# Performance work log

Measured on AMD Instinct MI355X. Metric: run time of the kernel, lower is better.

Reference implementation:

```python
import jax, jax.numpy as jnp
import numpy as np

B, K, D, H = 16, 256, 256, 128

def setup_inputs() -> dict:
    key = jax.random.key(0)
    k1, k2, k3 = jax.random.split(key, 3)
    x = jax.random.normal(k1, (B, K, D), dtype=jnp.float32)
    # Linear(2D, H): weight stored as (2D, H) for x @ W convention
    W1 = jax.random.normal(k2, (2 * D, H), dtype=jnp.float32) * (1.0 / np.sqrt(2 * D))
    b1 = jnp.zeros((H,), dtype=jnp.float32)
    W2 = jax.random.normal(k3, (H, D), dtype=jnp.float32) * (1.0 / np.sqrt(H))
    b2 = jnp.zeros((D,), dtype=jnp.float32)
    return {"x": x, "W1": W1, "b1": b1, "W2": W2, "b2": b2}

def reference(x, W1, b1, W2, b2):
    # Original: for each i, concat([x_i broadcast, x_j]) -> Linear -> ReLU -> Linear -> mean_j, + residual.
    # Split the first Linear over the concat: W1 = [W1a; W1b], so
    # pre-act(i,j) = x_i @ W1a + x_j @ W1b + b1  (avoids materializing the concat).
    D_ = x.shape[-1]
    W1a, W1b = W1[:D_], W1[D_:]
    a = jnp.einsum('bkd,dh->bkh', x, W1a)            # B x K x H (query side)
    b = jnp.einsum('bkd,dh->bkh', x, W1b)            # B x K x H (key side)
    h = jax.nn.relu(a[:, :, None, :] + b[:, None, :, :] + b1)  # B x K x K x H
    mh = h.mean(axis=2)                               # mean over j; Linear commutes with mean
    out = jnp.einsum('bkh,hd->bkd', mh, W2) + b2      # B x K x D
    return out + x
```

## Files before the change

### kernel.cpp

```cpp
#include <hip/hip_runtime.h>

typedef __attribute__((ext_vector_type(8))) short bf16x8;
typedef __attribute__((ext_vector_type(4))) float f32x4;

union FragU { uint4 q; bf16x8 h; };

__device__ __forceinline__ unsigned short f2bf(float f) {
  unsigned u = __float_as_uint(f);
  u += 0x7FFFu + ((u >> 16) & 1u);
  return (unsigned short)(u >> 16);
}
__device__ __forceinline__ unsigned pack2(float lo, float hi) {
  return (unsigned)f2bf(lo) | ((unsigned)f2bf(hi) << 16);
}

__global__ __launch_bounds__(256) void kX(
    const float* __restrict__ x, const float* __restrict__ W1,
    const float* __restrict__ W2, uint4* __restrict__ xbf,
    uint4* __restrict__ w1f, uint4* __restrict__ w2f)
{
  const int u = blockIdx.x * 256 + threadIdx.x;
  if (u < 131072) {
    const int l = u & 63, c = (u >> 6) & 7, t = (u >> 9) & 15, b = u >> 13;
    const int fr = l & 15, fq = l >> 4;
    const float* p = x + (size_t)((b * 16 + t) * 16 + fr) * 256 + c * 32 + fq * 8;
    float4 va = *(const float4*)p;
    float4 vb = *(const float4*)(p + 4);
    xbf[u] = make_uint4(pack2(va.x, va.y), pack2(va.z, va.w),
                        pack2(vb.x, vb.y), pack2(vb.z, vb.w));
  } else if (u < 139264) {
    const int u2 = u - 131072;
    const int l = u2 & 63, c = (u2 >> 6) & 7, hc = u2 >> 9;
    const int fr = l & 15, fq = l >> 4;
    const float* p = W1 + (size_t)((fr >= 8) ? 256 : 0) * 128 +
                     (size_t)(c * 32 + fq * 8) * 128 + hc * 8 + (fr & 7);
    float v[8];
#pragma unroll
    for (int j = 0; j < 8; ++j) v[j] = p[(size_t)j * 128];
    w1f[u2] = make_uint4(pack2(v[0], v[1]), pack2(v[2], v[3]),
                         pack2(v[4], v[5]), pack2(v[6], v[7]));
  } else if (u < 143360) {
    const int u3 = u - 139264;
    const int l = u3 & 63, c = (u3 >> 6) & 3, dg = u3 >> 8;
    const int fr = l & 15, fq = l >> 4;
    const float* p = W2 + (size_t)(c * 32 + fq * 8) * 256 + dg * 16 + fr;
    float v[8];
#pragma unroll
    for (int j = 0; j < 8; ++j) v[j] = p[(size_t)j * 256];
    w2f[u3] = make_uint4(pack2(v[0], v[1]), pack2(v[2], v[3]),
                         pack2(v[4], v[5]), pack2(v[6], v[7]));
  }
}

__global__ __launch_bounds__(1024) void kA(
    const uint4* __restrict__ xbf, const uint4* __restrict__ w1f,
    const float* __restrict__ b1, uint4* __restrict__ mf)
{
  __shared__ float Cs[8][260];
  __shared__ float As[8][260];
  __shared__ float PB[8][260];

  const int tid = threadIdx.x, lane = tid & 63, wv = tid >> 6;
  const int b = blockIdx.x, hc = blockIdx.y;
  const int fr = lane & 15, fq = lane >> 4;

  FragU afr[8];
#pragma unroll
  for (int c = 0; c < 8; ++c) afr[c].q = w1f[(hc * 8 + c) * 64 + lane];

  float b1v[4];
#pragma unroll
  for (int g = 0; g < 4; ++g)
    b1v[g] = (fq >= 2) ? b1[hc * 8 + (fq - 2) * 4 + g] : 0.f;

  {
    const int t = wv;
    f32x4 acc = {0.f, 0.f, 0.f, 0.f};
#pragma unroll
    for (int c = 0; c < 8; ++c) {
      FragU bfr;
      bfr.q = xbf[((size_t)(b * 16 + t) * 8 + c) * 64 + lane];
      acc = __builtin_amdgcn_mfma_f32_16x16x32_bf16(afr[c].h, bfr.h, acc, 0, 0, 0);
    }
    const int m = t * 16 + fr;
    if (fq < 2) {
#pragma unroll
      for (int g = 0; g < 4; ++g) As[fq * 4 + g][m] = acc[g];
    } else {
#pragma unroll
      for (int g = 0; g < 4; ++g) Cs[(fq - 2) * 4 + g][m] = acc[g] + b1v[g];
    }
  }
  __syncthreads();

  const int hp = wv & 7, kh = wv >> 3;
  const float a0 = As[hp][lane],       a1 = As[hp][64 + lane];
  const float a2 = As[hp][128 + lane], a3 = As[hp][192 + lane];

  float sumC = 0.f;
  if (kh == 0) {
    float4 s4 = *(const float4*)&Cs[hp][lane * 4];
    sumC = (s4.x + s4.y) + (s4.z + s4.w);
#pragma unroll
    for (int off = 32; off >= 1; off >>= 1) sumC += __shfl_xor(sumC, off, 64);
  }

  float s0a = 0.f, s0b = 0.f, s1a = 0.f, s1b = 0.f;
  float s2a = 0.f, s2b = 0.f, s3a = 0.f, s3b = 0.f;
  const int u0 = kh * 32;
#pragma unroll 8
  for (int u = 0; u < 32; ++u) {
    float4 c = *(const float4*)&Cs[hp][(u0 + u) * 4];
    s0a += fabsf(a0 + c.x); s0b += fabsf(a0 + c.y);
    s0a += fabsf(a0 + c.z); s0b += fabsf(a0 + c.w);
    s1a += fabsf(a1 + c.x); s1b += fabsf(a1 + c.y);
    s1a += fabsf(a1 + c.z); s1b += fabsf(a1 + c.w);
    s2a += fabsf(a2 + c.x); s2b += fabsf(a2 + c.y);
    s2a += fabsf(a2 + c.z); s2b += fabsf(a2 + c.w);
    s3a += fabsf(a3 + c.x); s3b += fabsf(a3 + c.y);
    s3a += fabsf(a3 + c.z); s3b += fabsf(a3 + c.w);
  }

  if (kh == 1) {
    PB[hp][lane]       = s0a + s0b;
    PB[hp][64 + lane]  = s1a + s1b;
    PB[hp][128 + lane] = s2a + s2b;
    PB[hp][192 + lane] = s3a + s3b;
  }
  __syncthreads();

  if (kh == 0) {
    As[hp][lane]       = (256.f * a0 + sumC + (s0a + s0b) + PB[hp][lane])       * (1.f / 512.f);
    As[hp][64 + lane]  = (256.f * a1 + sumC + (s1a + s1b) + PB[hp][64 + lane])  * (1.f / 512.f);
    As[hp][128 + lane] = (256.f * a2 + sumC + (s2a + s2b) + PB[hp][128 + lane]) * (1.f / 512.f);
    As[hp][192 + lane] = (256.f * a3 + sumC + (s3a + s3b) + PB[hp][192 + lane]) * (1.f / 512.f);
  }
  __syncthreads();

  if (tid < 256) {
    const int fr2 = tid & 15, T = tid >> 4;
    uint4 o = make_uint4(pack2(As[0][tid], As[1][tid]), pack2(As[2][tid], As[3][tid]),
                         pack2(As[4][tid], As[5][tid]), pack2(As[6][tid], As[7][tid]));
    mf[((size_t)(b * 16 + T) * 4 + (hc >> 2)) * 64 + (hc & 3) * 16 + fr2] = o;
  }
}

__global__ __launch_bounds__(256) void kB(
    const uint4* __restrict__ mf, const uint4* __restrict__ w2f,
    const float* __restrict__ b2, const float* __restrict__ x,
    float* __restrict__ out)
{
  const int tid = threadIdx.x, lane = tid & 63, wu = tid >> 6;
  const int mt = blockIdx.x;
  const int dg = blockIdx.y * 4 + wu;
  const int fr = lane & 15, fq = lane >> 4;

  f32x4 acc = {0.f, 0.f, 0.f, 0.f};
#pragma unroll
  for (int c = 0; c < 4; ++c) {
    FragU a, bb;
    a.q  = mf[((size_t)mt * 4 + c) * 64 + lane];
    bb.q = w2f[((size_t)dg * 4 + c) * 64 + lane];
    acc = __builtin_amdgcn_mfma_f32_16x16x32_bf16(a.h, bb.h, acc, 0, 0, 0);
  }

  const int d = dg * 16 + fr;
  const float bv = b2[d];
#pragma unroll
  for (int g = 0; g < 4; ++g) {
    const int m = mt * 16 + fq * 4 + g;
    const size_t o = (size_t)m * 256 + d;
    out[o] = acc[g] + bv + x[o];
  }
}

extern "C" void kernel_launch(void* const* d_in, const int* in_sizes, int n_in,
                              void* d_out, int out_size, void* d_ws, size_t ws_size,
                              hipStream_t stream) {
  const float* x  = (const float*)d_in[0];
  const float* W1 = (const float*)d_in[1];
  const float* b1 = (const float*)d_in[2];
  const float* W2 = (const float*)d_in[3];
  const float* b2 = (const float*)d_in[4];
  float* out = (float*)d_out;

  char* ws = (char*)d_ws;
  uint4* xbf = (uint4*)ws;
  uint4* w1f = (uint4*)(ws + (2u << 20));
  uint4* w2f = (uint4*)(ws + (2u << 20) + (128u << 10));
  uint4* mf  = (uint4*)(ws + (2u << 20) + (192u << 10));

  kX<<<560, 256, 0, stream>>>(x, W1, W2, xbf, w1f, w2f);
  kA<<<dim3(16, 16), 1024, 0, stream>>>(xbf, w1f, b1, mf);
  kB<<<dim3(256, 4), 256, 0, stream>>>(mf, w2f, b2, x, out);
}
```

Before: 25.60 us.

## Fuse bf16 conversion into consumer kernels and drop the pre-pass kernel

Removes the separate conversion kernel. kA now loads fp32 x for its batch, converts it with the hardware packed bf16 convert instruction, and stores it in a swizzled 128KB LDS tile. It also converts its W1 fragments directly from global memory, and kB converts its W2 fragments the same way. The goal is to cut one launch and the intermediate workspace round-trip. The cost is that each of the 16 hc blocks per batch re-reads and re-converts the full fp32 x slice, and the large LDS footprint limits occupancy. The pairwise abs-sum loop also switches to inline-asm packed f32 adds.

```diff
diff --git a/kernel.cpp b/kernel.cpp
--- a/kernel.cpp
+++ b/kernel.cpp
@@ -2,93 +2,73 @@
 
 typedef __attribute__((ext_vector_type(8))) short bf16x8;
 typedef __attribute__((ext_vector_type(4))) float f32x4;
+typedef __attribute__((ext_vector_type(2))) float f32x2;
 
 union FragU { uint4 q; bf16x8 h; };
 
-__device__ __forceinline__ unsigned short f2bf(float f) {
-  unsigned u = __float_as_uint(f);
-  u += 0x7FFFu + ((u >> 16) & 1u);
-  return (unsigned short)(u >> 16);
-}
-__device__ __forceinline__ unsigned pack2(float lo, float hi) {
-  return (unsigned)f2bf(lo) | ((unsigned)f2bf(hi) << 16);
-}
-
-__global__ __launch_bounds__(256) void kX(
-    const float* __restrict__ x, const float* __restrict__ W1,
-    const float* __restrict__ W2, uint4* __restrict__ xbf,
-    uint4* __restrict__ w1f, uint4* __restrict__ w2f)
-{
-  const int u = blockIdx.x * 256 + threadIdx.x;
-  if (u < 131072) {
-    const int l = u & 63, c = (u >> 6) & 7, t = (u >> 9) & 15, b = u >> 13;
-    const int fr = l & 15, fq = l >> 4;
-    const float* p = x + (size_t)((b * 16 + t) * 16 + fr) * 256 + c * 32 + fq * 8;
-    float4 va = *(const float4*)p;
-    float4 vb = *(const float4*)(p + 4);
-    xbf[u] = make_uint4(pack2(va.x, va.y), pack2(va.z, va.w),
-                        pack2(vb.x, vb.y), pack2(vb.z, vb.w));
-  } else if (u < 139264) {
-    const int u2 = u - 131072;
-    const int l = u2 & 63, c = (u2 >> 6) & 7, hc = u2 >> 9;
-    const int fr = l & 15, fq = l >> 4;
-    const float* p = W1 + (size_t)((fr >= 8) ? 256 : 0) * 128 +
-                     (size_t)(c * 32 + fq * 8) * 128 + hc * 8 + (fr & 7);
-    float v[8];
-#pragma unroll
-    for (int j = 0; j < 8; ++j) v[j] = p[(size_t)j * 128];
-    w1f[u2] = make_uint4(pack2(v[0], v[1]), pack2(v[2], v[3]),
-                         pack2(v[4], v[5]), pack2(v[6], v[7]));
-  } else if (u < 143360) {
-    const int u3 = u - 139264;
-    const int l = u3 & 63, c = (u3 >> 6) & 3, dg = u3 >> 8;
-    const int fr = l & 15, fq = l >> 4;
-    const float* p = W2 + (size_t)(c * 32 + fq * 8) * 256 + dg * 16 + fr;
-    float v[8];
-#pragma unroll
-    for (int j = 0; j < 8; ++j) v[j] = p[(size_t)j * 256];
-    w2f[u3] = make_uint4(pack2(v[0], v[1]), pack2(v[2], v[3]),
-                         pack2(v[4], v[5]), pack2(v[6], v[7]));
-  }
+__device__ __forceinline__ unsigned cvt_pk(float lo, float hi) {
+  unsigned r;
+  asm("v_cvt_pk_bf16_f32 %0, %1, %2" : "=v"(r) : "v"(lo), "v"(hi));
+  return r;
 }
 
 __global__ __launch_bounds__(1024) void kA(
-    const uint4* __restrict__ xbf, const uint4* __restrict__ w1f,
+    const float* __restrict__ x, const float* __restrict__ W1,
     const float* __restrict__ b1, uint4* __restrict__ mf)
 {
+  __shared__ __align__(16) unsigned short xs[256 * 256];
+  __shared__ float As[8][260];
   __shared__ float Cs[8][260];
-  __shared__ float As[8][260];
   __shared__ float PB[8][260];
 
   const int tid = threadIdx.x, lane = tid & 63, wv = tid >> 6;
   const int b = blockIdx.x, hc = blockIdx.y;
   const int fr = lane & 15, fq = lane >> 4;
 
+#pragma unroll
+  for (int i = 0; i < 16; ++i) {
+    const int idx = i * 1024 + tid;
+    const int row = idx >> 6, u = idx & 63;
+    float4 v = *(const float4*)&x[(size_t)(b * 256 + row) * 256 + u * 4];
+    uint2 hv = make_uint2(cvt_pk(v.x, v.y), cvt_pk(v.z, v.w));
+    *(uint2*)&xs[row * 256 + (u ^ ((row & 7) << 1)) * 4] = hv;
+  }
+
+  const float* __restrict__ wp =
+      W1 + (size_t)((fr >= 8) ? 256 : 0) * 128 + hc * 8 + (fr & 7);
   FragU afr[8];
 #pragma unroll
-  for (int c = 0; c < 8; ++c) afr[c].q = w1f[(hc * 8 + c) * 64 + lane];
+  for (int c = 0; c < 8; ++c) {
+    float v[8];
+#pragma unroll
+    for (int j = 0; j < 8; ++j) v[j] = wp[(size_t)(c * 32 + fq * 8 + j) * 128];
+    afr[c].q = make_uint4(cvt_pk(v[0], v[1]), cvt_pk(v[2], v[3]),
+                          cvt_pk(v[4], v[5]), cvt_pk(v[6], v[7]));
+  }
 
   float b1v[4];
 #pragma unroll
   for (int g = 0; g < 4; ++g)
     b1v[g] = (fq >= 2) ? b1[hc * 8 + (fq - 2) * 4 + g] : 0.f;
 
+  __syncthreads();
+
   {
-    const int t = wv;
+    const int mrow = wv * 16 + fr;
+    const int swz = (mrow & 7) << 1;
     f32x4 acc = {0.f, 0.f, 0.f, 0.f};
 #pragma unroll
     for (int c = 0; c < 8; ++c) {
-      FragU bfr;
-      bfr.q = xbf[((size_t)(b * 16 + t) * 8 + c) * 64 + lane];
-      acc = __builtin_amdgcn_mfma_f32_16x16x32_bf16(afr[c].h, bfr.h, acc, 0, 0, 0);
+      const int pu = (c * 8 + fq * 2) ^ swz;
+      bf16x8 bfr = *(const bf16x8*)&xs[mrow * 256 + pu * 4];
+      acc = __builtin_amdgcn_mfma_f32_16x16x32_bf16(afr[c].h, bfr, acc, 0, 0, 0);
     }
-    const int m = t * 16 + fr;
     if (fq < 2) {
 #pragma unroll
-      for (int g = 0; g < 4; ++g) As[fq * 4 + g][m] = acc[g];
+      for (int g = 0; g < 4; ++g) As[fq * 4 + g][mrow] = acc[g];
     } else {
 #pragma unroll
-      for (int g = 0; g < 4; ++g) Cs[(fq - 2) * 4 + g][m] = acc[g] + b1v[g];
+      for (int g = 0; g < 4; ++g) Cs[(fq - 2) * 4 + g][mrow] = acc[g] + b1v[g];
     }
   }
   __syncthreads();
@@ -105,48 +85,57 @@
     for (int off = 32; off >= 1; off >>= 1) sumC += __shfl_xor(sumC, off, 64);
   }
 
-  float s0a = 0.f, s0b = 0.f, s1a = 0.f, s1b = 0.f;
-  float s2a = 0.f, s2b = 0.f, s3a = 0.f, s3b = 0.f;
+  const f32x2 aa0 = {a0, a0}, aa1 = {a1, a1}, aa2 = {a2, a2}, aa3 = {a3, a3};
+  float s0l = 0.f, s0h = 0.f, s1l = 0.f, s1h = 0.f;
+  float s2l = 0.f, s2h = 0.f, s3l = 0.f, s3h = 0.f;
   const int u0 = kh * 32;
+
+#define PROW(aa, sl, sh)                                                   \
+  {                                                                        \
+    f32x2 t0, t1;                                                          \
+    asm("v_pk_add_f32 %0, %1, %2" : "=v"(t0) : "v"(aa), "v"(c01));         \
+    asm("v_pk_add_f32 %0, %1, %2" : "=v"(t1) : "v"(aa), "v"(c23));         \
+    sl += __builtin_fabsf(t0.x); sh += __builtin_fabsf(t0.y);              \
+    sl += __builtin_fabsf(t1.x); sh += __builtin_fabsf(t1.y);              \
+  }
+
 #pragma unroll 8
   for (int u = 0; u < 32; ++u) {
-    float4 c = *(const float4*)&Cs[hp][(u0 + u) * 4];
-    s0a += fabsf(a0 + c.x); s0b += fabsf(a0 + c.y);
-    s0a += fabsf(a0 + c.z); s0b += fabsf(a0 + c.w);
-    s1a += fabsf(a1 + c.x); s1b += fabsf(a1 + c.y);
-    s1a += fabsf(a1 + c.z); s1b += fabsf(a1 + c.w);
-    s2a += fabsf(a2 + c.x); s2b += fabsf(a2 + c.y);
-    s2a += fabsf(a2 + c.z); s2b += fabsf(a2 + c.w);
-    s3a += fabsf(a3 + c.x); s3b += fabsf(a3 + c.y);
-    s3a += fabsf(a3 + c.z); s3b += fabsf(a3 + c.w);
+    float4 c4 = *(const float4*)&Cs[hp][(u0 + u) * 4];
+    f32x2 c01 = {c4.x, c4.y}, c23 = {c4.z, c4.w};
+    PROW(aa0, s0l, s0h)
+    PROW(aa1, s1l, s1h)
+    PROW(aa2, s2l, s2h)
+    PROW(aa3, s3l, s3h)
   }
+#undef PROW
 
   if (kh == 1) {
-    PB[hp][lane]       = s0a + s0b;
-    PB[hp][64 + lane]  = s1a + s1b;
-    PB[hp][128 + lane] = s2a + s2b;
-    PB[hp][192 + lane] = s3a + s3b;
+    PB[hp][lane]       = s0l + s0h;
+    PB[hp][64 + lane]  = s1l + s1h;
+    PB[hp][128 + lane] = s2l + s2h;
+    PB[hp][192 + lane] = s3l + s3h;
   }
   __syncthreads();
 
   if (kh == 0) {
-    As[hp][lane]       = (256.f * a0 + sumC + (s0a + s0b) + PB[hp][lane])       * (1.f / 512.f);
-    As[hp][64 + lane]  = (256.f * a1 + sumC + (s1a + s1b) + PB[hp][64 + lane])  * (1.f / 512.f);
-    As[hp][128 + lane] = (256.f * a2 + sumC + (s2a + s2b) + PB[hp][128 + lane]) * (1.f / 512.f);
-    As[hp][192 + lane] = (256.f * a3 + sumC + (s3a + s3b) + PB[hp][192 + lane]) * (1.f / 512.f);
+    As[hp][lane]       = (256.f * a0 + sumC + (s0l + s0h) + PB[hp][lane])       * (1.f / 512.f);
+    As[hp][64 + lane]  = (256.f * a1 + sumC + (s1l + s1h) + PB[hp][64 + lane])  * (1.f / 512.f);
+    As[hp][128 + lane] = (256.f * a2 + sumC + (s2l + s2h) + PB[hp][128 + lane]) * (1.f / 512.f);
+    As[hp][192 + lane] = (256.f * a3 + sumC + (s3l + s3h) + PB[hp][192 + lane]) * (1.f / 512.f);
   }
   __syncthreads();
 
   if (tid < 256) {
     const int fr2 = tid & 15, T = tid >> 4;
-    uint4 o = make_uint4(pack2(As[0][tid], As[1][tid]), pack2(As[2][tid], As[3][tid]),
-                         pack2(As[4][tid], As[5][tid]), pack2(As[6][tid], As[7][tid]));
+    uint4 o = make_uint4(cvt_pk(As[0][tid], As[1][tid]), cvt_pk(As[2][tid], As[3][tid]),
+                         cvt_pk(As[4][tid], As[5][tid]), cvt_pk(As[6][tid], As[7][tid]));
     mf[((size_t)(b * 16 + T) * 4 + (hc >> 2)) * 64 + (hc & 3) * 16 + fr2] = o;
   }
 }
 
 __global__ __launch_bounds__(256) void kB(
-    const uint4* __restrict__ mf, const uint4* __restrict__ w2f,
+    const uint4* __restrict__ mf, const float* __restrict__ W2,
     const float* __restrict__ b2, const float* __restrict__ x,
     float* __restrict__ out)
 {
@@ -155,13 +144,23 @@
   const int dg = blockIdx.y * 4 + wu;
   const int fr = lane & 15, fq = lane >> 4;
 
+  const float* __restrict__ w2p = W2 + dg * 16 + fr;
+  FragU bfr[4];
+#pragma unroll
+  for (int c = 0; c < 4; ++c) {
+    float v[8];
+#pragma unroll
+    for (int j = 0; j < 8; ++j) v[j] = w2p[(size_t)(c * 32 + fq * 8 + j) * 256];
+    bfr[c].q = make_uint4(cvt_pk(v[0], v[1]), cvt_pk(v[2], v[3]),
+                          cvt_pk(v[4], v[5]), cvt_pk(v[6], v[7]));
+  }
+
   f32x4 acc = {0.f, 0.f, 0.f, 0.f};
 #pragma unroll
   for (int c = 0; c < 4; ++c) {
-    FragU a, bb;
-    a.q  = mf[((size_t)mt * 4 + c) * 64 + lane];
-    bb.q = w2f[((size_t)dg * 4 + c) * 64 + lane];
-    acc = __builtin_amdgcn_mfma_f32_16x16x32_bf16(a.h, bb.h, acc, 0, 0, 0);
+    FragU a;
+    a.q = mf[((size_t)mt * 4 + c) * 64 + lane];
+    acc = __builtin_amdgcn_mfma_f32_16x16x32_bf16(a.h, bfr[c].h, acc, 0, 0, 0);
   }
 
   const int d = dg * 16 + fr;
@@ -184,13 +183,8 @@
   const float* b2 = (const float*)d_in[4];
   float* out = (float*)d_out;
 
-  char* ws = (char*)d_ws;
-  uint4* xbf = (uint4*)ws;
-  uint4* w1f = (uint4*)(ws + (2u << 20));
-  uint4* w2f = (uint4*)(ws + (2u << 20) + (128u << 10));
-  uint4* mf  = (uint4*)(ws + (2u << 20) + (192u << 10));
+  uint4* mf = (uint4*)d_ws;
 
-  kX<<<560, 256, 0, stream>>>(x, W1, W2, xbf, w1f, w2f);
-  kA<<<dim3(16, 16), 1024, 0, stream>>>(xbf, w1f, b1, mf);
-  kB<<<dim3(256, 4), 256, 0, stream>>>(mf, w2f, b2, x, out);
+  kA<<<dim3(16, 16), 1024, 0, stream>>>(x, W1, b1, mf);
+  kB<<<dim3(256, 4), 256, 0, stream>>>(mf, W2, b2, x, out);
 }
```

New measurement: 25.91 us. No clear change (+1.2%).

## Replace pairwise ReLU mean with sort, suffix sums and binary search

Applied to the files above, without the earlier changes.

The O(K^2) per-channel sum of relu(a_i + c_j), which the old code evaluated as a sum of absolute values, is replaced by sorting the 256 key-side values with a wave-level bitonic sort and building suffix sums with a shuffle scan. Each query then binary-searches the sorted keys, and its mean becomes count*a plus the suffix sum, divided by 256. This turns about 256 adds per output into 8 LDS lookups, at the cost of sort and scan shuffles. Only 8 waves do the sort while the others sit idle, and the sum order changes, which slightly alters rounding.

```diff
diff --git a/kernel.cpp b/kernel.cpp
--- a/kernel.cpp
+++ b/kernel.cpp
@@ -58,7 +58,8 @@
 {
   __shared__ float Cs[8][260];
   __shared__ float As[8][260];
-  __shared__ float PB[8][260];
+  __shared__ float sortedC[8][256];
+  __shared__ float sufS[8][260];
 
   const int tid = threadIdx.x, lane = tid & 63, wv = tid >> 6;
   const int b = blockIdx.x, hc = blockIdx.y;
@@ -93,55 +94,88 @@
   }
   __syncthreads();
 
-  const int hp = wv & 7, kh = wv >> 3;
-  const float a0 = As[hp][lane],       a1 = As[hp][64 + lane];
-  const float a2 = As[hp][128 + lane], a3 = As[hp][192 + lane];
-
-  float sumC = 0.f;
-  if (kh == 0) {
-    float4 s4 = *(const float4*)&Cs[hp][lane * 4];
-    sumC = (s4.x + s4.y) + (s4.z + s4.w);
-#pragma unroll
-    for (int off = 32; off >= 1; off >>= 1) sumC += __shfl_xor(sumC, off, 64);
-  }
-
-  float s0a = 0.f, s0b = 0.f, s1a = 0.f, s1b = 0.f;
-  float s2a = 0.f, s2b = 0.f, s3a = 0.f, s3b = 0.f;
-  const int u0 = kh * 32;
-#pragma unroll 8
-  for (int u = 0; u < 32; ++u) {
-    float4 c = *(const float4*)&Cs[hp][(u0 + u) * 4];
-    s0a += fabsf(a0 + c.x); s0b += fabsf(a0 + c.y);
-    s0a += fabsf(a0 + c.z); s0b += fabsf(a0 + c.w);
-    s1a += fabsf(a1 + c.x); s1b += fabsf(a1 + c.y);
-    s1a += fabsf(a1 + c.z); s1b += fabsf(a1 + c.w);
-    s2a += fabsf(a2 + c.x); s2b += fabsf(a2 + c.y);
-    s2a += fabsf(a2 + c.z); s2b += fabsf(a2 + c.w);
-    s3a += fabsf(a3 + c.x); s3b += fabsf(a3 + c.y);
-    s3a += fabsf(a3 + c.z); s3b += fabsf(a3 + c.w);
-  }
-
-  if (kh == 1) {
-    PB[hp][lane]       = s0a + s0b;
-    PB[hp][64 + lane]  = s1a + s1b;
-    PB[hp][128 + lane] = s2a + s2b;
-    PB[hp][192 + lane] = s3a + s3b;
+  if (wv < 8) {
+    const int hp = wv;
+    float v0 = Cs[hp][lane * 4 + 0], v1 = Cs[hp][lane * 4 + 1];
+    float v2 = Cs[hp][lane * 4 + 2], v3 = Cs[hp][lane * 4 + 3];
+
+#define CE2(X, Y, UP)                                     \
+    {                                                     \
+      float mn = fminf(X, Y), mx = fmaxf(X, Y);           \
+      X = (UP) ? mn : mx;  Y = (UP) ? mx : mn;            \
+    }
+    CE2(v0, v1, true) CE2(v2, v3, false)
+    {
+      const bool up4 = (lane & 1) == 0;
+      CE2(v0, v2, up4) CE2(v1, v3, up4)
+      CE2(v0, v1, up4) CE2(v2, v3, up4)
+    }
+#pragma unroll
+    for (int k4 = 2; k4 <= 64; k4 <<= 1) {
+      const bool up = (lane & k4) == 0;
+#pragma unroll
+      for (int j4 = k4 >> 1; j4 >= 1; j4 >>= 1) {
+        const bool keepMin = (((lane & j4) == 0) == up);
+#define CEX(V)                                            \
+        {                                                 \
+          float o = __shfl_xor(V, j4, 64);                \
+          V = keepMin ? fminf(V, o) : fmaxf(V, o);        \
+        }
+        CEX(v0) CEX(v1) CEX(v2) CEX(v3)
+#undef CEX
+      }
+      CE2(v0, v2, up) CE2(v1, v3, up)
+      CE2(v0, v1, up) CE2(v2, v3, up)
+    }
+#undef CE2
+
+    const float sl = (v0 + v1) + (v2 + v3);
+    float inc = sl;
+#pragma unroll
+    for (int off = 1; off < 64; off <<= 1) {
+      float t = __shfl_down(inc, off, 64);
+      inc += (lane + off < 64) ? t : 0.f;
+    }
+    const float T = inc - sl;
+    const float su3 = T + v3;
+    const float su2 = su3 + v2;
+    const float su1 = su2 + v1;
+    const float su0 = su1 + v0;
+    sortedC[hp][lane * 4 + 0] = v0;
+    sortedC[hp][lane * 4 + 1] = v1;
+    sortedC[hp][lane * 4 + 2] = v2;
+    sortedC[hp][lane * 4 + 3] = v3;
+    sufS[hp][lane * 4 + 0] = su0;
+    sufS[hp][lane * 4 + 1] = su1;
+    sufS[hp][lane * 4 + 2] = su2;
+    sufS[hp][lane * 4 + 3] = su3;
+    if (lane == 0) sufS[hp][256] = 0.f;
   }
   __syncthreads();
 
-  if (kh == 0) {
-    As[hp][lane]       = (256.f * a0 + sumC + (s0a + s0b) + PB[hp][lane])       * (1.f / 512.f);
-    As[hp][64 + lane]  = (256.f * a1 + sumC + (s1a + s1b) + PB[hp][64 + lane])  * (1.f / 512.f);
-    As[hp][128 + lane] = (256.f * a2 + sumC + (s2a + s2b) + PB[hp][128 + lane]) * (1.f / 512.f);
-    As[hp][192 + lane] = (256.f * a3 + sumC + (s3a + s3b) + PB[hp][192 + lane]) * (1.f / 512.f);
+  {
+    const int hp = wv & 7, half = wv >> 3;
+#pragma unroll
+    for (int q = 0; q < 2; ++q) {
+      const int m = half * 128 + q * 64 + lane;
+      const float a = As[hp][m];
+      const float t = -a;
+      int idx = 0;
+#pragma unroll
+      for (int st = 128; st >= 1; st >>= 1)
+        idx += (sortedC[hp][idx + st - 1] <= t) ? st : 0;
+      const float cnt = (float)(256 - idx);
+      const float S = sufS[hp][idx];
+      As[hp][m] = (cnt * a + S) * (1.f / 256.f);
+    }
   }
   __syncthreads();
 
   if (tid < 256) {
-    const int fr2 = tid & 15, T = tid >> 4;
+    const int fr2 = tid & 15, T2 = tid >> 4;
     uint4 o = make_uint4(pack2(As[0][tid], As[1][tid]), pack2(As[2][tid], As[3][tid]),
                          pack2(As[4][tid], As[5][tid]), pack2(As[6][tid], As[7][tid]));
-    mf[((size_t)(b * 16 + T) * 4 + (hc >> 2)) * 64 + (hc & 3) * 16 + fr2] = o;
+    mf[((size_t)(b * 16 + T2) * 4 + (hc >> 2)) * 64 + (hc & 3) * 16 + fr2] = o;
   }
 }
 
```

Result: faster. 21.50 us (median of 2 runs) (-16.0%).
